# Performance work log

Measured on AMD Instinct MI355X. Metric: run time of the kernel, lower is better.

## Reference

```python
import jax, jax.numpy as jnp
import numpy as np

B, S, H = 1, 2048, 768
NH, HD, NF = 12, 64, 128
ALPHA = 0.9
SIGMA = 1.0
EPS_NORM = 1e-5


def setup_inputs() -> dict:
    key = jax.random.key(0)
    ks = jax.random.split(key, 12)
    s = 1.0 / np.sqrt(H)
    inp = {
        "hidden_states": jax.random.normal(ks[0], (B, S, H), dtype=jnp.float32),
        "attention_mask": jnp.ones((B, 1, 1, S), dtype=jnp.float32),
        "Wq": jax.random.normal(ks[1], (H, H), dtype=jnp.float32) * s,
        "bq": jnp.zeros((H,), dtype=jnp.float32),
        "Wk": jax.random.normal(ks[2], (H, H), dtype=jnp.float32) * s,
        "bk": jnp.zeros((H,), dtype=jnp.float32),
        "Wv": jax.random.normal(ks[3], (H, H), dtype=jnp.float32) * s,
        "bv": jnp.zeros((H,), dtype=jnp.float32),
        "Wo": jax.random.normal(ks[4], (H, H), dtype=jnp.float32) * s,
        "bo": jnp.zeros((H,), dtype=jnp.float32),
        # per-head RFF params: omega ~ N(0, I), bias ~ U[0, 2pi]
        "omega": jax.random.normal(ks[5], (NH, NF, HD), dtype=jnp.float32),
        "rff_b": jax.random.uniform(ks[6], (NH, NF), dtype=jnp.float32, maxval=2.0 * np.pi),
    }
    return inp


def _phi(x, omega, rff_b):
    # x: (b, h, s, d) -> RFF features (b, h, s, f)
    z = jnp.einsum("bhsd,hfd->bhsf", x, omega) / SIGMA + rff_b[None, :, None, :]
    phi = jnp.sqrt(2.0 / NF) * jnp.cos(z)
    # normalize=True: L2-normalize feature vectors
    phi = phi / (jnp.linalg.norm(phi, axis=-1, keepdims=True) + 1e-6)
    return phi


def reference(hidden_states, attention_mask, Wq, bq, Wk, bk, Wv, bv, Wo, bo, omega, rff_b):
    b, s, _ = hidden_states.shape

    def proj(W, bias):
        y = jnp.einsum("bsh,oh->bso", hidden_states, W) + bias
        return y.reshape(b, s, NH, HD).transpose(0, 2, 1, 3)  # (b,h,s,d)

    q = proj(Wq, bq)
    k = proj(Wk, bk)
    v = proj(Wv, bv)

    dot_scores = jnp.einsum("bhsd,bhtd->bhst", q, k) / jnp.sqrt(jnp.float32(HD))

    qn = q / (jnp.linalg.norm(q, axis=-1, keepdims=True) + EPS_NORM)
    kn = k / (jnp.linalg.norm(k, axis=-1, keepdims=True) + EPS_NORM)
    phi_q = _phi(qn, omega, rff_b)
    phi_k = _phi(kn, omega, rff_b)
    kernel_scores = jnp.einsum("bhsf,bhtf->bhst", phi_q, phi_k)

    scores = ALPHA * dot_scores + (1.0 - ALPHA) * kernel_scores
    scores = scores + (attention_mask - 1.0) * 10000.0

    weights = jax.nn.softmax(scores, axis=-1)  # dropout is identity in eval
    context = jnp.einsum("bhst,bhtd->bhsd", weights, v)
    context = context.transpose(0, 2, 1, 3).reshape(b, s, H)
    output = jnp.einsum("bsh,oh->bso", context, Wo) + bo
    return output, weights
```

## Files before the change

### kernel.cpp

```cpp
#include <hip/hip_runtime.h>
#include <cmath>

#define TS 2048
#define TH 768
#define TNH 12
#define THD 64
#define TNF 128
#define KC 192

typedef __attribute__((ext_vector_type(4))) short s16x4;
typedef __attribute__((ext_vector_type(8))) short short8;
typedef __attribute__((ext_vector_type(8))) __bf16 bf16x8;
typedef __attribute__((ext_vector_type(4))) float floatx4;

__device__ __forceinline__ short f2bf(float x) {
    union { float f; unsigned u; } v; v.f = x;
    unsigned r = v.u + 0x7FFFu + ((v.u >> 16) & 1u);
    return (short)(r >> 16);
}
__device__ __forceinline__ float bf2f(short x) {
    union { unsigned u; float f; } v;
    v.u = ((unsigned)(unsigned short)x) << 16;
    return v.f;
}

__device__ __forceinline__ float waveReduceSum(float v) {
#pragma unroll
    for (int off = 32; off >= 1; off >>= 1) v += __shfl_xor(v, off, 64);
    return v;
}
__device__ __forceinline__ float waveReduceMax(float v) {
#pragma unroll
    for (int off = 32; off >= 1; off >>= 1) v = fmaxf(v, __shfl_xor(v, off, 64));
    return v;
}

__device__ __forceinline__ void fma16(float (&acc)[4][4], const float* pa, const float* pb) {
#pragma unroll
    for (int kk = 0; kk < 32; ++kk) {
        float4 a = *(const float4*)(pa + kk * 68);
        float4 b = *(const float4*)(pb + kk * 68);
        float av[4] = {a.x, a.y, a.z, a.w};
        float bv[4] = {b.x, b.y, b.z, b.w};
#pragma unroll
        for (int i = 0; i < 4; ++i)
#pragma unroll
            for (int j = 0; j < 4; ++j) acc[i][j] += av[i] * bv[j];
    }
}

__global__ __launch_bounds__(256) void k_proj_qkv(
    const float* __restrict__ X,
    const float* __restrict__ W0, const float* __restrict__ b0,
    const float* __restrict__ W1, const float* __restrict__ b1,
    const float* __restrict__ W2, const float* __restrict__ b2,
    float* __restrict__ dq, float* __restrict__ dk, short* __restrict__ Vb,
    short* __restrict__ Qc, short* __restrict__ Kc) {
    __shared__ float As[32][68];
    __shared__ float Bs[32][68];
    const int z = blockIdx.z;
    const float* W = (z == 0) ? W0 : ((z == 1) ? W1 : W2);
    const float* bias = (z == 0) ? b0 : ((z == 1) ? b1 : b2);
    float* dst = (z == 0) ? dq : dk;
    const int n0 = blockIdx.x * 64;
    const int m0 = blockIdx.y * 64;
    const int tid = threadIdx.x;
    float acc[4][4] = {};
    for (int k0 = 0; k0 < TH; k0 += 32) {
#pragma unroll
        for (int l = 0; l < 2; ++l) {
            int i = tid + l * 256;
            int row = i >> 3, col = (i & 7) << 2;
            float4 a = *(const float4*)&X[(m0 + row) * TH + k0 + col];
            As[col + 0][row] = a.x; As[col + 1][row] = a.y;
            As[col + 2][row] = a.z; As[col + 3][row] = a.w;
            float4 b = *(const float4*)&W[(n0 + row) * TH + k0 + col];
            Bs[col + 0][row] = b.x; Bs[col + 1][row] = b.y;
            Bs[col + 2][row] = b.z; Bs[col + 3][row] = b.w;
        }
        __syncthreads();
        fma16(acc, &As[0][0] + ((tid >> 4) << 2), &Bs[0][0] + ((tid & 15) << 2));
        __syncthreads();
    }
    const int mb = m0 + ((tid >> 4) << 2);
    const int nb = n0 + ((tid & 15) << 2);
    if (z == 2) {
#pragma unroll
        for (int j = 0; j < 4; ++j) {
            int n = nb + j;
            int h = n >> 6, d = n & 63;
            float bv = bias[n];
            s16x4 pk;
#pragma unroll
            for (int i = 0; i < 4; ++i) pk[i] = f2bf(acc[i][j] + bv);
            *(s16x4*)&Vb[(size_t)(h * THD + d) * TS + mb] = pk;
        }
    } else {
#pragma unroll
        for (int i = 0; i < 4; ++i)
#pragma unroll
            for (int j = 0; j < 4; ++j) {
                int n = nb + j;
                float val = acc[i][j] + bias[n];
                int h = n >> 6, d = n & 63;
                int row = h * TS + (mb + i);
                dst[row * THD + d] = val;
                if (z == 0) Qc[(size_t)row * KC + d] = f2bf(val * 0.1125f);
                else Kc[(size_t)row * KC + d] = f2bf(val);
            }
    }
}

__global__ __launch_bounds__(256) void k_proj_out(
    const float* __restrict__ X, const float* __restrict__ W,
    const float* __restrict__ bias, float* __restrict__ out) {
    __shared__ float As[32][68];
    __shared__ float Bs[32][68];
    const int n0 = blockIdx.x * 64;
    const int m0 = blockIdx.y * 64;
    const int tid = threadIdx.x;
    float acc[4][4] = {};
    for (int k0 = 0; k0 < TH; k0 += 32) {
#pragma unroll
        for (int l = 0; l < 2; ++l) {
            int i = tid + l * 256;
            int row = i >> 3, col = (i & 7) << 2;
            float4 a = *(const float4*)&X[(m0 + row) * TH + k0 + col];
            As[col + 0][row] = a.x; As[col + 1][row] = a.y;
            As[col + 2][row] = a.z; As[col + 3][row] = a.w;
            float4 b = *(const float4*)&W[(n0 + row) * TH + k0 + col];
            Bs[col + 0][row] = b.x; Bs[col + 1][row] = b.y;
            Bs[col + 2][row] = b.z; Bs[col + 3][row] = b.w;
        }
        __syncthreads();
        fma16(acc, &As[0][0] + ((tid >> 4) << 2), &Bs[0][0] + ((tid & 15) << 2));
        __syncthreads();
    }
    const int mb = m0 + ((tid >> 4) << 2);
    const int nb = n0 + ((tid & 15) << 2);
#pragma unroll
    for (int i = 0; i < 4; ++i)
#pragma unroll
        for (int j = 0; j < 4; ++j) {
            int n = nb + j;
            out[(mb + i) * TH + n] = acc[i][j] + bias[n];
        }
}

__global__ __launch_bounds__(64) void k_rownorm(
    const float* __restrict__ q, const float* __restrict__ kbuf,
    float* __restrict__ invq, float* __restrict__ invk) {
    const int row = blockIdx.x;
    const float* src = blockIdx.y ? kbuf : q;
    float* dst = blockIdx.y ? invk : invq;
    float x = src[row * THD + threadIdx.x];
    float ss = waveReduceSum(x * x);
    if (threadIdx.x == 0) dst[row] = 1.0f / (sqrtf(ss) + 1e-5f);
}

__global__ __launch_bounds__(256) void k_phi(
    const float* __restrict__ q, const float* __restrict__ kbuf,
    const float* __restrict__ invq, const float* __restrict__ invk,
    const float* __restrict__ omega, const float* __restrict__ rffb,
    short* __restrict__ Qc, short* __restrict__ Kc) {
    __shared__ float As[32][68];
    __shared__ float Bs[32][68];
    const int z = blockIdx.z;
    const int h = z >> 1, which = z & 1;
    const float* X = which ? kbuf : q;
    const float* inv = which ? invk : invq;
    short* dst = which ? Kc : Qc;
    const int n0 = blockIdx.x * 64;
    const int m0 = blockIdx.y * 64;
    const int tid = threadIdx.x;
    float acc[4][4] = {};
    for (int k0 = 0; k0 < THD; k0 += 32) {
#pragma unroll
        for (int l = 0; l < 2; ++l) {
            int i = tid + l * 256;
            int row = i >> 3, col = (i & 7) << 2;
            int rq = h * TS + m0 + row;
            float s = inv[rq];
            float4 a = *(const float4*)&X[rq * THD + k0 + col];
            As[col + 0][row] = a.x * s; As[col + 1][row] = a.y * s;
            As[col + 2][row] = a.z * s; As[col + 3][row] = a.w * s;
            float4 b = *(const float4*)&omega[(h * TNF + n0 + row) * THD + k0 + col];
            Bs[col + 0][row] = b.x; Bs[col + 1][row] = b.y;
            Bs[col + 2][row] = b.z; Bs[col + 3][row] = b.w;
        }
        __syncthreads();
        fma16(acc, &As[0][0] + ((tid >> 4) << 2), &Bs[0][0] + ((tid & 15) << 2));
        __syncthreads();
    }
    const int mb = m0 + ((tid >> 4) << 2);
    const int nb = n0 + ((tid & 15) << 2);
#pragma unroll
    for (int i = 0; i < 4; ++i)
#pragma unroll
        for (int j = 0; j < 4; ++j) {
            int f = nb + j;
            float zv = acc[i][j] + rffb[h * TNF + f];
            dst[(size_t)(h * TS + (mb + i)) * KC + 64 + f] = f2bf(0.125f * cosf(zv));
        }
}

__global__ __launch_bounds__(128) void k_phinorm(short* __restrict__ Qc, short* __restrict__ Kc) {
    const int row = blockIdx.x;
    short* buf = (blockIdx.y ? Kc : Qc) + (size_t)row * KC + 64;
    const float scale0 = blockIdx.y ? 1.0f : 0.1f;
    const int tid = threadIdx.x;
    float p = bf2f(buf[tid]);
    float ss = waveReduceSum(p * p);
    __shared__ float sh[2];
    if ((tid & 63) == 0) sh[tid >> 6] = ss;
    __syncthreads();
    ss = sh[0] + sh[1];
    float sc = scale0 / (sqrtf(ss) + 1e-6f);
    buf[tid] = f2bf(p * sc);
}

__global__ __launch_bounds__(256) void k_scores_mfma(
    const short* __restrict__ Qc, const short* __restrict__ Kc,
    const float* __restrict__ mask, float* __restrict__ wout) {
    __shared__ __align__(16) short Asb[128][40];
    __shared__ __align__(16) short Bsb[128][40];
    const int h = blockIdx.z;
    const int n0 = blockIdx.x * 128;
    const int m0 = blockIdx.y * 128;
    const int tid = threadIdx.x;
    const int lane = tid & 63;
    const int w = tid >> 6;
    const int wm = (w >> 1) * 64, wn = (w & 1) * 64;
    const int fr = lane & 15;
    const int quad = lane >> 4;

    floatx4 acc[4][4] = {};

    for (int k0 = 0; k0 < KC; k0 += 32) {
#pragma unroll
        for (int l = 0; l < 2; ++l) {
            int c = tid + l * 256;
            int row = c >> 2, col = (c & 3) << 3;
            short8 a = *(const short8*)&Qc[(size_t)(h * TS + m0 + row) * KC + k0 + col];
            *(short8*)&Asb[row][col] = a;
            short8 b = *(const short8*)&Kc[(size_t)(h * TS + n0 + row) * KC + k0 + col];
            *(short8*)&Bsb[row][col] = b;
        }
        __syncthreads();
        bf16x8 af[4], bfr[4];
#pragma unroll
        for (int i = 0; i < 4; ++i) af[i] = *(const bf16x8*)&Asb[wm + i * 16 + fr][quad * 8];
#pragma unroll
        for (int j = 0; j < 4; ++j) bfr[j] = *(const bf16x8*)&Bsb[wn + j * 16 + fr][quad * 8];
#pragma unroll
        for (int i = 0; i < 4; ++i)
#pragma unroll
            for (int j = 0; j < 4; ++j)
                acc[i][j] = __builtin_amdgcn_mfma_f32_16x16x32_bf16(af[i], bfr[j], acc[i][j], 0, 0, 0);
        __syncthreads();
    }
#pragma unroll
    for (int j = 0; j < 4; ++j) {
        int col_g = n0 + wn + j * 16 + fr;
        float mb = (mask[col_g] - 1.0f) * 10000.0f;
#pragma unroll
        for (int i = 0; i < 4; ++i) {
#pragma unroll
            for (int r = 0; r < 4; ++r) {
                int row_g = m0 + wm + i * 16 + quad * 4 + r;
                wout[(size_t)(h * TS + row_g) * TS + col_g] = acc[i][j][r] + mb;
            }
        }
    }
}

__global__ __launch_bounds__(256) void k_softmax(float* __restrict__ wout) {
    const int row = blockIdx.x;
    float4* p = (float4*)(wout + (size_t)row * TS);
    const int tid = threadIdx.x;
    float4 x0 = p[tid], x1 = p[tid + 256];
    float mx = fmaxf(fmaxf(fmaxf(x0.x, x0.y), fmaxf(x0.z, x0.w)),
                     fmaxf(fmaxf(x1.x, x1.y), fmaxf(x1.z, x1.w)));
    mx = waveReduceMax(mx);
    __shared__ float rm[4];
    __shared__ float rs[4];
    if ((tid & 63) == 0) rm[tid >> 6] = mx;
    __syncthreads();
    mx = fmaxf(fmaxf(rm[0], rm[1]), fmaxf(rm[2], rm[3]));
    float e[8];
    e[0] = __expf(x0.x - mx); e[1] = __expf(x0.y - mx);
    e[2] = __expf(x0.z - mx); e[3] = __expf(x0.w - mx);
    e[4] = __expf(x1.x - mx); e[5] = __expf(x1.y - mx);
    e[6] = __expf(x1.z - mx); e[7] = __expf(x1.w - mx);
    float sum = ((e[0] + e[1]) + (e[2] + e[3])) + ((e[4] + e[5]) + (e[6] + e[7]));
    sum = waveReduceSum(sum);
    if ((tid & 63) == 0) rs[tid >> 6] = sum;
    __syncthreads();
    sum = rs[0] + rs[1] + rs[2] + rs[3];
    float rinv = 1.0f / sum;
    x0.x = e[0] * rinv; x0.y = e[1] * rinv; x0.z = e[2] * rinv; x0.w = e[3] * rinv;
    x1.x = e[4] * rinv; x1.y = e[5] * rinv; x1.z = e[6] * rinv; x1.w = e[7] * rinv;
    p[tid] = x0;
    p[tid + 256] = x1;
}

__global__ __launch_bounds__(256) void k_ctx_mfma(
    const float* __restrict__ wout, const short* __restrict__ Vb, float* __restrict__ ctx) {
    __shared__ __align__(16) short Asb[128][40];
    __shared__ __align__(16) short Bsb[64][40];
    const int h = blockIdx.y;
    const int m0 = blockIdx.x * 128;
    const int tid = threadIdx.x;
    const int lane = tid & 63;
    const int w = tid >> 6;
    const int wm = w * 32;
    const int fr = lane & 15;
    const int quad = lane >> 4;
    floatx4 acc[2][4] = {};
    for (int k0 = 0; k0 < TS; k0 += 32) {
#pragma unroll
        for (int l = 0; l < 4; ++l) {
            int idx = tid + l * 256;
            int row = idx >> 3, col = (idx & 7) << 2;
            float4 a = *(const float4*)&wout[(size_t)(h * TS + m0 + row) * TS + k0 + col];
            s16x4 s;
            s[0] = f2bf(a.x); s[1] = f2bf(a.y); s[2] = f2bf(a.z); s[3] = f2bf(a.w);
            *(s16x4*)&Asb[row][col] = s;
        }
        {
            int row = tid >> 2, col = (tid & 3) << 3;
            *(short8*)&Bsb[row][col] =
                *(const short8*)&Vb[(size_t)(h * THD + row) * TS + k0 + col];
        }
        __syncthreads();
        bf16x8 af[2], bfr[4];
#pragma unroll
        for (int i = 0; i < 2; ++i) af[i] = *(const bf16x8*)&Asb[wm + i * 16 + fr][quad * 8];
#pragma unroll
        for (int j = 0; j < 4; ++j) bfr[j] = *(const bf16x8*)&Bsb[j * 16 + fr][quad * 8];
#pragma unroll
        for (int i = 0; i < 2; ++i)
#pragma unroll
            for (int j = 0; j < 4; ++j)
                acc[i][j] = __builtin_amdgcn_mfma_f32_16x16x32_bf16(af[i], bfr[j], acc[i][j], 0, 0, 0);
        __syncthreads();
    }
#pragma unroll
    for (int i = 0; i < 2; ++i)
#pragma unroll
        for (int j = 0; j < 4; ++j)
#pragma unroll
            for (int r = 0; r < 4; ++r) {
                int row_g = m0 + wm + i * 16 + quad * 4 + r;
                ctx[(size_t)row_g * TH + h * THD + j * 16 + fr] = acc[i][j][r];
            }
}

extern "C" void kernel_launch(void* const* d_in, const int* in_sizes, int n_in,
                              void* d_out, int out_size, void* d_ws, size_t ws_size,
                              hipStream_t stream) {
    const float* hs    = (const float*)d_in[0];
    const float* mask  = (const float*)d_in[1];
    const float* Wq    = (const float*)d_in[2];
    const float* bq    = (const float*)d_in[3];
    const float* Wk    = (const float*)d_in[4];
    const float* bk    = (const float*)d_in[5];
    const float* Wv    = (const float*)d_in[6];
    const float* bv    = (const float*)d_in[7];
    const float* Wo    = (const float*)d_in[8];
    const float* bo    = (const float*)d_in[9];
    const float* omega = (const float*)d_in[10];
    const float* rffb  = (const float*)d_in[11];

    float* out0 = (float*)d_out;
    float* wout = out0 + TS * TH;

    float* ws   = (float*)d_ws;
    float* q    = ws;
    float* kbuf = ws + 1572864;
    short* Vb   = (short*)(ws + 3145728);
    float* invq = ws + 4718592;
    float* invk = ws + 4743168;
    float* ctx  = ws + 4767744;
    short* Qc   = (short*)(ws + 6340608);
    short* Kc   = (short*)(ws + 8699904);

    k_proj_qkv<<<dim3(12, 32, 3), 256, 0, stream>>>(hs, Wq, bq, Wk, bk, Wv, bv, q, kbuf, Vb, Qc, Kc);
    k_rownorm<<<dim3(TNH * TS, 2), 64, 0, stream>>>(q, kbuf, invq, invk);
    k_phi<<<dim3(2, 32, 24), 256, 0, stream>>>(q, kbuf, invq, invk, omega, rffb, Qc, Kc);
    k_phinorm<<<dim3(TNH * TS, 2), 128, 0, stream>>>(Qc, Kc);
    k_scores_mfma<<<dim3(16, 16, 12), 256, 0, stream>>>(Qc, Kc, mask, wout);
    k_softmax<<<TNH * TS, 256, 0, stream>>>(wout);
    k_ctx_mfma<<<dim3(16, 12), 256, 0, stream>>>(wout, Vb, ctx);
    k_proj_out<<<dim3(12, 32), 256, 0, stream>>>(ctx, Wo, bo, out0);
}
```

Baseline: 598.5 us.

## Convert QKV projection to bf16 MFMA with pre-converted inputs

```diff
diff --git a/kernel.cpp b/kernel.cpp
--- a/kernel.cpp
+++ b/kernel.cpp
@@ -49,65 +49,102 @@
     }
 }
 
-__global__ __launch_bounds__(256) void k_proj_qkv(
-    const float* __restrict__ X,
-    const float* __restrict__ W0, const float* __restrict__ b0,
-    const float* __restrict__ W1, const float* __restrict__ b1,
-    const float* __restrict__ W2, const float* __restrict__ b2,
+__global__ __launch_bounds__(256) void k_cvt_bf16(
+    const float* __restrict__ s0, const float* __restrict__ s1,
+    const float* __restrict__ s2, const float* __restrict__ s3,
+    short* __restrict__ d0, short* __restrict__ d1,
+    short* __restrict__ d2, short* __restrict__ d3) {
+    const int y = blockIdx.y;
+    const float* src = (y == 0) ? s0 : ((y == 1) ? s1 : ((y == 2) ? s2 : s3));
+    short* dst = (y == 0) ? d0 : ((y == 1) ? d1 : ((y == 2) ? d2 : d3));
+    const int n4 = (y == 0) ? (TS * TH / 4) : (TH * TH / 4);
+    for (int i = blockIdx.x * 256 + threadIdx.x; i < n4; i += gridDim.x * 256) {
+        float4 v = ((const float4*)src)[i];
+        s16x4 o;
+        o[0] = f2bf(v.x); o[1] = f2bf(v.y); o[2] = f2bf(v.z); o[3] = f2bf(v.w);
+        *(s16x4*)&dst[i * 4] = o;
+    }
+}
+
+__global__ __launch_bounds__(256) void k_proj_qkv_mfma(
+    const short* __restrict__ Xb,
+    const short* __restrict__ Wqb, const short* __restrict__ Wkb, const short* __restrict__ Wvb,
+    const float* __restrict__ b0, const float* __restrict__ b1, const float* __restrict__ b2,
     float* __restrict__ dq, float* __restrict__ dk, short* __restrict__ Vb,
     short* __restrict__ Qc, short* __restrict__ Kc) {
-    __shared__ float As[32][68];
-    __shared__ float Bs[32][68];
+    __shared__ __align__(16) short Asb[128][40];
+    __shared__ __align__(16) short Bsb[128][40];
     const int z = blockIdx.z;
-    const float* W = (z == 0) ? W0 : ((z == 1) ? W1 : W2);
+    const short* W = (z == 0) ? Wqb : ((z == 1) ? Wkb : Wvb);
     const float* bias = (z == 0) ? b0 : ((z == 1) ? b1 : b2);
-    float* dst = (z == 0) ? dq : dk;
-    const int n0 = blockIdx.x * 64;
-    const int m0 = blockIdx.y * 64;
-    const int tid = threadIdx.x;
-    float acc[4][4] = {};
+    const int n0 = blockIdx.x * 128;
+    const int m0 = blockIdx.y * 128;
+    const int tid = threadIdx.x;
+    const int lane = tid & 63;
+    const int w = tid >> 6;
+    const int wm = (w >> 1) * 64, wn = (w & 1) * 64;
+    const int fr = lane & 15;
+    const int quad = lane >> 4;
+
+    floatx4 acc[4][4] = {};
+
     for (int k0 = 0; k0 < TH; k0 += 32) {
 #pragma unroll
         for (int l = 0; l < 2; ++l) {
-            int i = tid + l * 256;
-            int row = i >> 3, col = (i & 7) << 2;
-            float4 a = *(const float4*)&X[(m0 + row) * TH + k0 + col];
-            As[col + 0][row] = a.x; As[col + 1][row] = a.y;
-            As[col + 2][row] = a.z; As[col + 3][row] = a.w;
-            float4 b = *(const float4*)&W[(n0 + row) * TH + k0 + col];
-            Bs[col + 0][row] = b.x; Bs[col + 1][row] = b.y;
-            Bs[col + 2][row] = b.z; Bs[col + 3][row] = b.w;
-        }
-        __syncthreads();
-        fma16(acc, &As[0][0] + ((tid >> 4) << 2), &Bs[0][0] + ((tid & 15) << 2));
-        __syncthreads();
-    }
-    const int mb = m0 + ((tid >> 4) << 2);
-    const int nb = n0 + ((tid & 15) << 2);
+            int c = tid + l * 256;
+            int row = c >> 2, col = (c & 3) << 3;
+            *(short8*)&Asb[row][col] = *(const short8*)&Xb[(size_t)(m0 + row) * TH + k0 + col];
+            *(short8*)&Bsb[row][col] = *(const short8*)&W[(size_t)(n0 + row) * TH + k0 + col];
+        }
+        __syncthreads();
+        bf16x8 af[4], bfr[4];
+#pragma unroll
+        for (int i = 0; i < 4; ++i) af[i] = *(const bf16x8*)&Asb[wm + i * 16 + fr][quad * 8];
+#pragma unroll
+        for (int j = 0; j < 4; ++j) bfr[j] = *(const bf16x8*)&Bsb[wn + j * 16 + fr][quad * 8];
+#pragma unroll
+        for (int i = 0; i < 4; ++i)
+#pragma unroll
+            for (int j = 0; j < 4; ++j)
+                acc[i][j] = __builtin_amdgcn_mfma_f32_16x16x32_bf16(af[i], bfr[j], acc[i][j], 0, 0, 0);
+        __syncthreads();
+    }
     if (z == 2) {
 #pragma unroll
         for (int j = 0; j < 4; ++j) {
-            int n = nb + j;
+            int n = n0 + wn + j * 16 + fr;
             int h = n >> 6, d = n & 63;
             float bv = bias[n];
-            s16x4 pk;
-#pragma unroll
-            for (int i = 0; i < 4; ++i) pk[i] = f2bf(acc[i][j] + bv);
-            *(s16x4*)&Vb[(size_t)(h * THD + d) * TS + mb] = pk;
+#pragma unroll
+            for (int i = 0; i < 4; ++i) {
+                int t = m0 + wm + i * 16 + quad * 4;
+                s16x4 pk;
+#pragma unroll
+                for (int r = 0; r < 4; ++r) pk[r] = f2bf(acc[i][j][r] + bv);
+                *(s16x4*)&Vb[(size_t)(h * THD + d) * TS + t] = pk;
+            }
         }
     } else {
-#pragma unroll
-        for (int i = 0; i < 4; ++i)
-#pragma unroll
-            for (int j = 0; j < 4; ++j) {
-                int n = nb + j;
-                float val = acc[i][j] + bias[n];
-                int h = n >> 6, d = n & 63;
-                int row = h * TS + (mb + i);
-                dst[row * THD + d] = val;
-                if (z == 0) Qc[(size_t)row * KC + d] = f2bf(val * 0.1125f);
-                else Kc[(size_t)row * KC + d] = f2bf(val);
+        float* dst = z ? dk : dq;
+        short* cc = z ? Kc : Qc;
+        const float qs = z ? 1.0f : 0.1125f;
+#pragma unroll
+        for (int j = 0; j < 4; ++j) {
+            int n = n0 + wn + j * 16 + fr;
+            int h = n >> 6, d = n & 63;
+            float bv = bias[n];
+#pragma unroll
+            for (int i = 0; i < 4; ++i) {
+#pragma unroll
+                for (int r = 0; r < 4; ++r) {
+                    int m = m0 + wm + i * 16 + quad * 4 + r;
+                    float val = acc[i][j][r] + bv;
+                    size_t rowi = (size_t)(h * TS + m);
+                    dst[rowi * THD + d] = val;
+                    cc[rowi * KC + d] = f2bf(val * qs);
+                }
             }
+        }
     }
 }
 
@@ -385,7 +422,14 @@
     short* Qc   = (short*)(ws + 6340608);
     short* Kc   = (short*)(ws + 8699904);
 
-    k_proj_qkv<<<dim3(12, 32, 3), 256, 0, stream>>>(hs, Wq, bq, Wk, bk, Wv, bv, q, kbuf, Vb, Qc, Kc);
+    short* Xb  = (short*)wout;
+    short* Wqb = Xb + (size_t)TS * TH;
+    short* Wkb = Wqb + (size_t)TH * TH;
+    short* Wvb = Wkb + (size_t)TH * TH;
+
+    k_cvt_bf16<<<dim3(512, 4), 256, 0, stream>>>(hs, Wq, Wk, Wv, Xb, Wqb, Wkb, Wvb);
+    k_proj_qkv_mfma<<<dim3(6, 16, 3), 256, 0, stream>>>(Xb, Wqb, Wkb, Wvb, bq, bk, bv,
+                                                        q, kbuf, Vb, Qc, Kc);
     k_rownorm<<<dim3(TNH * TS, 2), 64, 0, stream>>>(q, kbuf, invq, invk);
     k_phi<<<dim3(2, 32, 24), 256, 0, stream>>>(q, kbuf, invq, invk, omega, rffb, Qc, Kc);
     k_phinorm<<<dim3(TNH * TS, 2), 128, 0, stream>>>(Qc, Kc);
```

Result: faster. 504.0 us (-15.8%).
